# Performance work log

Hardware: AMD Instinct MI355X
Metric: run time of the kernel (lower is better)

The kernel has to match this reference:

```python
import jax, jax.numpy as jnp
import numpy as np

N_HEAD = 4
N_BIT = 8      # ssm coder bits, table_len = 2**8 = 256
IN_DIM = 8
FFN_V = 4      # ffn coder bits, 2**4 = 16 codes per head
FFN_DEPTH = 8  # tree depth, 2**8 = 256 leaves
TBL = 2 ** N_BIT


def _bern(key, logits):
    # torch.bernoulli(logits.sigmoid())
    return jax.random.uniform(key, logits.shape) < jax.nn.sigmoid(logits)


def _bool2long(x, n):
    mul = (2 ** (n - 1 - jnp.arange(n))).astype(jnp.int32)
    return (x.astype(jnp.int32) * mul).sum(-1)


def _long2bool(x, n):
    mul = (2 ** (n - 1 - jnp.arange(n))).astype(jnp.int32)
    return ((x[..., None] // mul) % 2).astype(bool)


def _tree_ffn(q, qs, key_p, val_p, rng):
    # q: (N, Q) bool, qs: (N, Q) float  (qs broadcast per head, matching intent)
    N, Q = q.shape
    H, depth = N_HEAD, FFN_DEPTH
    nv = 2 ** depth
    nk = nv - 1
    qf = jnp.broadcast_to(q[:, None, :], (N, H, Q)).reshape(N * H, Q)
    qs = jnp.broadcast_to(qs[:, None, :], (N, H, Q)).reshape(N * H, Q)
    qs = (2.0 * qf.astype(qs.dtype) - 1.0) * qs
    ix_h = jnp.arange(N * H, dtype=jnp.int32) % H
    ix = jnp.zeros(N * H, dtype=jnp.int32)
    key_flat = key_p.reshape(-1, 2 * Q)  # (H*nk, 2Q)
    support = None
    for d in range(depth):
        ix_k = ix_h * nk + (2 ** d - 1) + ix
        kw = key_flat[ix_k]  # (NH, 2Q)
        kb = _bern(jax.random.fold_in(rng, d), kw).reshape(-1, Q, 2)
        k1 = kb[:, :, 0].astype(qs.dtype)
        k2 = kb[:, :, 1].astype(qs.dtype)
        k1 = -jnp.logaddexp(-k1, qs)
        k2 = -jnp.logaddexp(-k2, -qs)
        lor_s = jnp.logaddexp(k1, k2)
        lor_s = -jax.nn.logsumexp(-lor_s, axis=-1)  # (NH,)
        lor = _bern(jax.random.fold_in(rng, 100 + d), lor_s)
        lor_s = (2.0 * lor.astype(qs.dtype) - 1.0) * lor_s
        ix = 2 * ix + lor.astype(jnp.int32)
        support = lor_s if support is None else -jnp.logaddexp(-support, -lor_s)
    vw = val_p.reshape(-1, val_p.shape[-1])[ix_h * nv + ix]  # (NH, V)
    vb = _bern(jax.random.fold_in(rng, 999), vw)
    vs = (2.0 * vb.astype(qs.dtype) - 1.0) * vw
    vs = -jnp.logaddexp(-vs, -support[:, None])
    return vb.reshape(N, H, -1), vs.reshape(N, H, -1)


def _forward(x, xs, ffn_key, ffn_value, table, state0):
    rng = jax.random.key(42)
    B, L, D = x.shape
    H, V, T = N_HEAD, FFN_V, TBL
    xb, xss = _tree_ffn(x.reshape(-1, D), xs.reshape(-1, D), ffn_key, ffn_value,
                        jax.random.fold_in(rng, 1))
    xb = xb.reshape(B, L, H, V)
    xss = xss.reshape(B, L, H, V)
    xcode = _bool2long(xb, V)                      # (B,L,H) in [0,16)
    xss = -jax.nn.logsumexp(-xss, axis=-1)         # (B,L,H)
    # sample stochastic lookup tables, independently per batch element
    tlog = jnp.broadcast_to(table, (B,) + table.shape[1:])  # (B,64,T,8)
    tb = _bern(jax.random.fold_in(rng, 2), tlog)
    table_s = table * (2.0 * tb.astype(xs.dtype) - 1.0)
    tcode = _bool2long(tb, N_BIT)                  # (B,64,T) in [0,T)
    table_s = -jax.nn.logsumexp(-table_s, axis=-1) # (B,64,T)
    head_off = (jnp.arange(L * H, dtype=jnp.int32) % H) * (2 ** V)
    idx = xcode.reshape(B, L * H) + head_off[None, :]
    y = jnp.take_along_axis(tcode, idx[:, :, None], axis=1).reshape(B, L, H, T)
    ys = jnp.take_along_axis(table_s, idx[:, :, None], axis=1).reshape(B, L, H, T)
    ys = -jnp.logaddexp(-ys, -xss[..., None])
    # Blelloch-style doubling scan; compose = table gather + soft-AND in log domain
    i = 1
    while i < L:
        y1 = y[:, :L - i]
        z = jnp.take_along_axis(y[:, i:], y1, axis=-1)
        zs = -jnp.logaddexp(-ys[:, :L - i], -jnp.take_along_axis(ys[:, i:], y1, axis=-1))
        y = jnp.concatenate([y[:, :i], z], axis=1)
        ys = jnp.concatenate([ys[:, :i], zs], axis=1)
        i *= 2
    # initial state
    s0b = _bern(jax.random.fold_in(rng, 3), jnp.broadcast_to(state0, (B,) + state0.shape[1:]))
    s0s = state0 * (2.0 * s0b.astype(xs.dtype) - 1.0)  # (B,H,8)
    s0 = _bool2long(s0b, N_BIT)                        # (B,H)
    s0s = -jax.nn.logsumexp(-s0s, axis=-1)             # (B,H)
    sidx = jnp.broadcast_to(s0[:, None, :, None], (B, L, H, 1))
    z = jnp.take_along_axis(y, sidx, axis=-1)[..., 0]   # (B,L,H)
    zs = jnp.take_along_axis(ys, sidx, axis=-1)[..., 0]
    zs = -jnp.logaddexp(-s0s[:, None, :], -zs)
    zb = _long2bool(z, N_BIT)                           # (B,L,H,8)
    zs = jnp.broadcast_to(zs[..., None], zb.shape)
    return zb.reshape(B, L, H * N_BIT), zs.reshape(B, L, H * N_BIT)


def setup_inputs() -> dict:
    key = jax.random.key(0)
    k = jax.random.split(key, 6)
    B, L = 8, 4096
    x = jax.random.randint(k[0], (B, L, IN_DIM), 0, 2).astype(bool)
    xs = jax.random.normal(k[1], (B, L, IN_DIM), dtype=jnp.float32)
    ffn_key = jax.random.normal(k[2], (N_HEAD, 2 ** FFN_DEPTH - 1, 2 * IN_DIM), dtype=jnp.float32) + 3.0
    ffn_value = jax.random.normal(k[3], (N_HEAD, 2 ** FFN_DEPTH, FFN_V), dtype=jnp.float32) + 3.0
    table = jax.random.normal(k[4], (1, (2 ** FFN_V) * N_HEAD, TBL, N_BIT), dtype=jnp.float32)
    state0 = jax.random.normal(k[5], (1, N_HEAD, N_BIT), dtype=jnp.float32)
    return {"x": x, "xs": xs, "ffn_key": ffn_key, "ffn_value": ffn_value,
            "table": table, "state0": state0}


def reference(x, xs, ffn_key, ffn_value, table, state0):
    return _forward(x, xs, ffn_key, ffn_value, table, state0)
```

## Files before the change

### kernel.cpp

```cpp
#include <hip/hip_runtime.h>
#include <hip/hip_bf16.h>
#include <stdint.h>
#include <math.h>

#define BB 8
#define LL 4096
#define HH 4
#define DD 8
#define VV 4
#define DEPTH 8
#define TBLN 256
#define NBIT 8
#define NROW 131072
#define CHUNK 64
#define NCHUNK 64

#define PARTITIONABLE 1
#define MATH_XLA_CPU 1

__device__ __forceinline__ uint32_t rotl32(uint32_t v, int r){ return (v<<r)|(v>>(32-r)); }

__device__ __forceinline__ void tf2x32(uint32_t k0, uint32_t k1, uint32_t x0, uint32_t x1,
                                       uint32_t& o0, uint32_t& o1){
  uint32_t ks2 = k0 ^ k1 ^ 0x1BD11BDAu;
  x0 += k0; x1 += k1;
  x0+=x1; x1=rotl32(x1,13); x1^=x0;
  x0+=x1; x1=rotl32(x1,15); x1^=x0;
  x0+=x1; x1=rotl32(x1,26); x1^=x0;
  x0+=x1; x1=rotl32(x1, 6); x1^=x0;
  x0+=k1; x1+=ks2+1u;
  x0+=x1; x1=rotl32(x1,17); x1^=x0;
  x0+=x1; x1=rotl32(x1,29); x1^=x0;
  x0+=x1; x1=rotl32(x1,16); x1^=x0;
  x0+=x1; x1=rotl32(x1,24); x1^=x0;
  x0+=ks2; x1+=k0+2u;
  x0+=x1; x1=rotl32(x1,13); x1^=x0;
  x0+=x1; x1=rotl32(x1,15); x1^=x0;
  x0+=x1; x1=rotl32(x1,26); x1^=x0;
  x0+=x1; x1=rotl32(x1, 6); x1^=x0;
  x0+=k0; x1+=k1+3u;
  x0+=x1; x1=rotl32(x1,17); x1^=x0;
  x0+=x1; x1=rotl32(x1,29); x1^=x0;
  x0+=x1; x1=rotl32(x1,16); x1^=x0;
  x0+=x1; x1=rotl32(x1,24); x1^=x0;
  x0+=k1; x1+=ks2+4u;
  x0+=x1; x1=rotl32(x1,13); x1^=x0;
  x0+=x1; x1=rotl32(x1,15); x1^=x0;
  x0+=x1; x1=rotl32(x1,26); x1^=x0;
  x0+=x1; x1=rotl32(x1, 6); x1^=x0;
  x0+=ks2; x1+=k0+5u;
  o0 = x0; o1 = x1;
}

struct K2 { uint32_t a, b; };
__device__ __forceinline__ K2 kfold(K2 k, uint32_t d){
  K2 r; tf2x32(k.a, k.b, 0u, d, r.a, r.b); return r;
}

__device__ __forceinline__ uint32_t rbits(K2 k, uint32_t p, uint32_t n){
#if PARTITIONABLE
  uint32_t o0, o1; tf2x32(k.a, k.b, 0u, p, o0, o1); return o0 ^ o1;
#else
  uint32_t half = n >> 1;
  uint32_t o0, o1;
  if (p < half){ tf2x32(k.a, k.b, p, p + half, o0, o1); return o0; }
  else         { tf2x32(k.a, k.b, p - half, p, o0, o1); return o1; }
#endif
}

__device__ __forceinline__ float bits2u(uint32_t b){
  return __uint_as_float((b >> 9) | 0x3f800000u) - 1.0f;
}

__device__ __forceinline__ float xla_expf(float x){
#if MATH_XLA_CPU
  #pragma clang fp contract(off)
  const float exp_hi = 88.3762626647950f;
  const float exp_lo = -88.3762626647949f;
  const float log2e  = 1.44269504088896341f;
  const float c1 = 0.693359375f;
  const float c2 = -2.12194440e-4f;
  float xc = fmaxf(fminf(x, exp_hi), exp_lo);
  float fx = floorf(xc * log2e + 0.5f);
  float tmp = fx * c1;
  float z1  = fx * c2;
  float r = xc - tmp;
  r = r - z1;
  float z = r * r;
  float y = 1.9875691500E-4f;
  y = y * r + 1.3981999507E-3f;
  y = y * r + 8.3334519073E-3f;
  y = y * r + 4.1665795894E-2f;
  y = y * r + 1.6666665459E-1f;
  y = y * r + 5.0000001201E-1f;
  y = y * z + r;
  y = y + 1.0f;
  int emm0 = (int)fx + 127;
  float scale = __int_as_float(emm0 << 23);
  return fmaxf(y * scale, x);
#else
  return expf(x);
#endif
}

__device__ __forceinline__ float xla_logf(float a){
#if MATH_XLA_CPU
  #pragma clang fp contract(off)
  float x = fmaxf(a, __uint_as_float(0x00800000u));
  uint32_t bits = __float_as_uint(x);
  int em = (int)(bits >> 23) - 126;
  x = __uint_as_float((bits & 0x007fffffu) | 0x3f000000u);
  float e = (float)em;
  bool mlt = x < 0.707106781186547524f;
  float tmp1 = mlt ? x : 0.0f;
  float xm = x - 1.0f;
  e = e - (mlt ? 1.0f : 0.0f);
  xm = xm + tmp1;
  float z = xm * xm;
  float y = 7.0376836292E-2f;
  y = y * xm + (-1.1514610310E-1f);
  y = y * xm + 1.1676998740E-1f;
  y = y * xm + (-1.2420140846E-1f);
  y = y * xm + 1.4249322787E-1f;
  y = y * xm + (-1.6668057665E-1f);
  y = y * xm + 2.0000714765E-1f;
  y = y * xm + (-2.4999993993E-1f);
  y = y * xm + 3.3333331174E-1f;
  y = y * xm;
  y = y * z;
  y = e * (-2.12194440e-4f) + y;
  y = y - 0.5f * z;
  float res = xm + y;
  res = e * 0.693359375f + res;
  return res;
#else
  return logf(a);
#endif
}

__device__ __forceinline__ float xla_log1pf(float x){
#if MATH_XLA_CPU
  #pragma clang fp contract(off)
  if (fabsf(x) < 1e-4f){
    return ((-0.5f * x) + 1.0f) * x;
  }
  return xla_logf(1.0f + x);
#else
  return log1pf(x);
#endif
}

__device__ __forceinline__ float xla_logaddexp(float a, float b){
  #pragma clang fp contract(off)
  float m = fmaxf(a, b);
  float d = a - b;
  return m + xla_log1pf(xla_expf(-fabsf(d)));
}

template<int NV>
__device__ __forceinline__ float neg_lse_neg(const float* v){
  #pragma clang fp contract(off)
  float m = -v[0];
  #pragma unroll
  for (int i = 1; i < NV; i++) m = fmaxf(m, -v[i]);
  float s = 0.f;
  #pragma unroll
  for (int i = 0; i < NV; i++) s = s + xla_expf((-v[i]) - m);
  return -(xla_logf(s) + m);
}

__device__ __forceinline__ bool bern_bit(float u, float w){
  #pragma clang fp contract(off)
  float e = xla_expf(-w);
  float s = 1.0f / (1.0f + e);
  return u < s;
}

__device__ __forceinline__ float andf(float a, float b){
  float na = -a, nb = -b;
  float m = fmaxf(na, nb);
  float d = fabsf(na - nb);
  return -(m + log1pf(expf(-d)));
}
#define AND_IDENT 1e30f

__global__ void k_init(const uint32_t* xw, int* flag,
                       const float* s0w, int* s0code, float* s0s){
  __shared__ int any;
  if (threadIdx.x == 0) any = 0;
  __syncthreads();
  int bad = 0;
  for (int i = threadIdx.x; i < 1024; i += 256){
    uint32_t w = xw[i];
    if (w != 0u && w != 1u && w != 0x3F800000u) bad = 1;
  }
  if (bad) atomicOr(&any, 1);
  __syncthreads();
  if (threadIdx.x == 0) *flag = any;

  int t = threadIdx.x;
  if (t < 32){
    int b = t >> 2, h = t & 3;
    K2 root{0u, 42u};
    K2 sk = kfold(root, 3u);
    float v[NBIT];
    uint32_t code = 0;
    #pragma unroll
    for (int j = 0; j < NBIT; j++){
      float w = s0w[h*NBIT + j];
      uint32_t p = (uint32_t)((b*4 + h)*NBIT + j);
      float u = bits2u(rbits(sk, p, 256u));
      bool bit = bern_bit(u, w);
      code |= (bit ? 1u : 0u) << (NBIT - 1 - j);
      v[j] = bit ? w : -w;
    }
    s0code[t] = (int)code;
    s0s[t]    = neg_lse_neg<NBIT>(v);
  }
}

__global__ __launch_bounds__(256) void k_ffn(const void* xraw, const float* xs,
                                             const float* fk, const float* fv,
                                             uint8_t* xcode, float* xss, const int* flag){
  int r = blockIdx.x * blockDim.x + threadIdx.x;
  if (r >= NROW) return;
  int n = r >> 2;
  int h = r & 3;
  bool u8mode = (*flag != 0);
  const uint8_t* x8   = (const uint8_t*)xraw;
  const uint32_t* x32 = (const uint32_t*)xraw;

  float qs[DD];
  #pragma unroll
  for (int j = 0; j < DD; j++){
    bool qb = u8mode ? (x8[n*DD + j] != 0) : (x32[n*DD + j] != 0u);
    float v = xs[n*DD + j];
    qs[j] = qb ? v : -v;
  }

  K2 root{0u, 42u};
  K2 rngT = kfold(root, 1u);

  uint32_t ix = 0;
  float support = 0.f;
  for (int d = 0; d < DEPTH; d++){
    K2 kd = kfold(rngT, (uint32_t)d);
    const float* kw = fk + (size_t)(h*255 + (1<<d) - 1 + (int)ix) * 16;
    float lor[DD];
    #pragma unroll
    for (int j = 0; j < DD; j++){
      uint32_t p1 = (uint32_t)r * 16u + 2u*(uint32_t)j;
      float u1 = bits2u(rbits(kd, p1,      2097152u));
      float u2 = bits2u(rbits(kd, p1 + 1u, 2097152u));
      float b1 = bern_bit(u1, kw[2*j])     ? 1.f : 0.f;
      float b2 = bern_bit(u2, kw[2*j + 1]) ? 1.f : 0.f;
      float k1 = -xla_logaddexp(-b1,  qs[j]);
      float k2 = -xla_logaddexp(-b2, -qs[j]);
      lor[j] = xla_logaddexp(k1, k2);
    }
    float lor_s = neg_lse_neg<DD>(lor);
    K2 lk = kfold(rngT, 100u + (uint32_t)d);
    float ul = bits2u(rbits(lk, (uint32_t)r, 131072u));
    bool lb = bern_bit(ul, lor_s);
    float ls = lb ? lor_s : -lor_s;
    ix = 2u*ix + (lb ? 1u : 0u);
    support = (d == 0) ? ls : -xla_logaddexp(-support, -ls);
  }

  K2 vk = kfold(rngT, 999u);
  const float* vw = fv + (size_t)(h*256 + (int)ix) * VV;
  float vs[VV];
  uint32_t code = 0;
  #pragma unroll
  for (int c = 0; c < VV; c++){
    float u = bits2u(rbits(vk, (uint32_t)r*4u + (uint32_t)c, 524288u));
    bool b = bern_bit(u, vw[c]);
    code |= (b ? 1u : 0u) << (VV - 1 - c);
    float sv = b ? vw[c] : -vw[c];
    vs[c] = -xla_logaddexp(-sv, -support);
  }
  xcode[r] = (uint8_t)code;
  xss[r]   = neg_lse_neg<VV>(vs);
}

__global__ __launch_bounds__(256) void k_table(const float* table, uint8_t* tcode, float* tabs){
  int idx = blockIdx.x * blockDim.x + threadIdx.x;
  if (idx >= 131072) return;
  int rem = idx & 16383;
  K2 root{0u, 42u};
  K2 tk = kfold(root, 2u);
  float v[NBIT];
  uint32_t code = 0;
  #pragma unroll
  for (int j = 0; j < NBIT; j++){
    float w = table[(size_t)rem * NBIT + j];
    uint32_t p = (uint32_t)idx * 8u + (uint32_t)j;
    float u = bits2u(rbits(tk, p, 1048576u));
    bool bit = bern_bit(u, w);
    code |= (bit ? 1u : 0u) << (NBIT - 1 - j);
    v[j] = bit ? w : -w;
  }
  tcode[idx] = (uint8_t)code;
  tabs[idx]  = neg_lse_neg<NBIT>(v);
}

__global__ __launch_bounds__(256) void k_A(const uint8_t* tcode, const uint8_t* xcode,
                                           uint8_t* F){
  int blk = blockIdx.x;
  int c  = blk & 63;
  int bh = blk >> 6;
  int b = bh >> 2, h = bh & 3;
  __shared__ int4 sT4[256];
  __shared__ uint8_t sXC[CHUNK];
  uint8_t* sT = (uint8_t*)sT4;
  int t = threadIdx.x;
  const int rowbase = (b*64 + h*16) * 256;
  sT4[t] = ((const int4*)(tcode + rowbase))[t];
  if (t < CHUNK){
    int l = c*CHUNK + t;
    sXC[t] = xcode[(b*LL + l)*HH + h];
  }
  __syncthreads();
  int cur = t;
  #pragma unroll 8
  for (int k = 0; k < CHUNK; k++){
    cur = sT[(int)sXC[k]*256 + cur];
  }
  F[(size_t)blk*256 + t] = (uint8_t)cur;
}

__global__ __launch_bounds__(256) void k_B(const uint8_t* F, const int* s0code, int* carryZ){
  int bh = blockIdx.x;
  __shared__ int4 sF4[1024];
  uint8_t* sF = (uint8_t*)sF4;
  int t = threadIdx.x;
  const int4* src = (const int4*)(F + (size_t)bh*16384);
  for (int i = t; i < 1024; i += 256) sF4[i] = src[i];
  __syncthreads();
  if (t == 0){
    int z = s0code[bh];
    for (int c = 0; c < NCHUNK; c++){ carryZ[bh*NCHUNK + c] = z; z = sF[c*256 + z]; }
  }
}

__global__ __launch_bounds__(64) void k_C1(const uint8_t* tcode, const float* tabs,
                                           const uint8_t* xcode, const float* xss,
                                           const int* carryZ,
                                           uint8_t* zOut, float* P, float* T){
  int blk = blockIdx.x;
  int c  = blk & 63;
  int bh = blk >> 6;
  int b = bh >> 2, h = bh & 3;
  __shared__ int4 sT4[256];
  uint8_t* sT = (uint8_t*)sT4;
  int t = threadIdx.x;
  const int rowbase = (b*64 + h*16) * 256;
  const int4* src = (const int4*)(tcode + rowbase);
  #pragma unroll
  for (int i = 0; i < 4; i++) sT4[t + 64*i] = src[t + 64*i];

  int l = c*CHUNK + t;
  int r = (b*LL + l)*HH + h;
  int   xcv = xcode[r];
  float xsv = xss[r];
  __syncthreads();

  int z = carryZ[blk];
  int aReg = 0, zReg = 0;
  for (int k = 0; k < CHUNK; k++){
    int xck = __shfl(xcv, k, 64);
    int a = xck*256 + z;
    z = sT[a];
    if (t == k){ aReg = a; zReg = z; }
  }

  float p = andf(tabs[rowbase + aReg], xsv);
  #pragma unroll
  for (int off = 1; off < 64; off <<= 1){
    float o = __shfl_up(p, off, 64);
    if (t >= off) p = andf(o, p);
  }
  zOut[blk*CHUNK + t] = (uint8_t)zReg;
  P[blk*CHUNK + t] = p;
  if (t == 63) T[blk] = p;
}

__global__ __launch_bounds__(256) void k_C2(const uint8_t* zOut, const float* P,
                                            const float* T, const float* s0s,
                                            float* out){
  int blk = blockIdx.x;
  int c = blk & 63;
  int b = blk >> 6;
  __shared__ float carryL[4];
  int t = threadIdx.x;
  int w = t >> 6, lane = t & 63;

  float val = (lane < c) ? T[(b*4 + w)*64 + lane] : AND_IDENT;
  #pragma unroll
  for (int off = 1; off < 64; off <<= 1){
    float o = __shfl_xor(val, off, 64);
    val = andf(val, o);
  }
  float carry = andf(val, s0s[b*4 + w]);
  if (lane == 0) carryL[w] = carry;
  __syncthreads();

  int k = t >> 2, h = t & 3;
  int cblk = (b*4 + h)*64 + c;
  int z = zOut[cblk*CHUNK + k];
  float sc = andf(carryL[h], P[cblk*CHUNK + k]);

  size_t base = (size_t)blk*2048 + (size_t)t*8;
  float4 b0, b1;
  b0.x = (float)((z >> 7) & 1); b0.y = (float)((z >> 6) & 1);
  b0.z = (float)((z >> 5) & 1); b0.w = (float)((z >> 4) & 1);
  b1.x = (float)((z >> 3) & 1); b1.y = (float)((z >> 2) & 1);
  b1.z = (float)((z >> 1) & 1); b1.w = (float)( z       & 1);
  float4 s4; s4.x = sc; s4.y = sc; s4.z = sc; s4.w = sc;
  *(float4*)(out + base)     = b0;
  *(float4*)(out + base + 4) = b1;
  *(float4*)(out + 1048576 + base)     = s4;
  *(float4*)(out + 1048576 + base + 4) = s4;
}

extern "C" void kernel_launch(void* const* d_in, const int* in_sizes, int n_in,
                              void* d_out, int out_size, void* d_ws, size_t ws_size,
                              hipStream_t stream) {
  const void*  x      = d_in[0];
  const float* xs     = (const float*)d_in[1];
  const float* fk     = (const float*)d_in[2];
  const float* fv     = (const float*)d_in[3];
  const float* table  = (const float*)d_in[4];
  const float* s0w    = (const float*)d_in[5];
  float* out          = (float*)d_out;

  uint8_t* ws = (uint8_t*)d_ws;
  uint8_t* xcode_ = ws;
  uint8_t* tcode_ = ws + 131072;
  uint8_t* F_     = ws + 262144;
  float*   xss_   = (float*)(ws + 786432);
  float*   tabs_  = (float*)(ws + 1310720);
  uint8_t* zOut_  = ws + 1835008;
  float*   P_     = (float*)(ws + 1966080);
  float*   T_     = (float*)(ws + 2490368);
  int*     carryZ_= (int*)  (ws + 2498560);
  int*     s0code_= (int*)  (ws + 2506752);
  float*   s0s_   = (float*)(ws + 2506880);
  int*     flag_  = (int*)  (ws + 2507008);

  k_init <<<1, 256, 0, stream>>>((const uint32_t*)x, flag_, s0w, s0code_, s0s_);
  k_ffn  <<<NROW/256, 256, 0, stream>>>(x, xs, fk, fv, xcode_, xss_, flag_);
  k_table<<<131072/256, 256, 0, stream>>>(table, tcode_, tabs_);
  k_A    <<<32*NCHUNK, 256, 0, stream>>>(tcode_, xcode_, F_);
  k_B    <<<32, 256, 0, stream>>>(F_, s0code_, carryZ_);
  k_C1   <<<32*NCHUNK, 64, 0, stream>>>(tcode_, tabs_, xcode_, xss_, carryZ_, zOut_, P_, T_);
  k_C2   <<<BB*NCHUNK, 256, 0, stream>>>(zOut_, P_, T_, s0s_, out);
}
```

Measured before the change: 204.7 us.

## Precompute sigmoids, RNG keys and per-bit logaddexp tables outside the tree loop

A new pre-pass kernel computes sigmoid of the table, ffn_key and ffn_value weights once, and derives the per-depth threefry fold keys once into a small buffer. The tree FFN precomputes, per input position, the four possible lor values (key bits 0/1 x 0/1), so each depth step only selects among them instead of evaluating three logaddexps per element. The table kernel uses vectorized float4 loads and compares against the precomputed sigmoids. This removes repeated exp/log and hash work in the hot kernels, at the cost of extra workspace traffic and one extra pass over the table.

```diff
diff --git a/kernel.cpp b/kernel.cpp
--- a/kernel.cpp
+++ b/kernel.cpp
@@ -9,7 +9,6 @@
 #define DD 8
 #define VV 4
 #define DEPTH 8
-#define TBLN 256
 #define NBIT 8
 #define NROW 131072
 #define CHUNK 64
@@ -57,14 +56,9 @@
   K2 r; tf2x32(k.a, k.b, 0u, d, r.a, r.b); return r;
 }
 
-__device__ __forceinline__ uint32_t rbits(K2 k, uint32_t p, uint32_t n){
+__device__ __forceinline__ uint32_t rbits(K2 k, uint32_t p){
 #if PARTITIONABLE
   uint32_t o0, o1; tf2x32(k.a, k.b, 0u, p, o0, o1); return o0 ^ o1;
-#else
-  uint32_t half = n >> 1;
-  uint32_t o0, o1;
-  if (p < half){ tf2x32(k.a, k.b, p, p + half, o0, o1); return o0; }
-  else         { tf2x32(k.a, k.b, p - half, p, o0, o1); return o1; }
 #endif
 }
 
@@ -73,7 +67,6 @@
 }
 
 __device__ __forceinline__ float xla_expf(float x){
-#if MATH_XLA_CPU
   #pragma clang fp contract(off)
   const float exp_hi = 88.3762626647950f;
   const float exp_lo = -88.3762626647949f;
@@ -98,13 +91,9 @@
   int emm0 = (int)fx + 127;
   float scale = __int_as_float(emm0 << 23);
   return fmaxf(y * scale, x);
-#else
-  return expf(x);
-#endif
 }
 
 __device__ __forceinline__ float xla_logf(float a){
-#if MATH_XLA_CPU
   #pragma clang fp contract(off)
   float x = fmaxf(a, __uint_as_float(0x00800000u));
   uint32_t bits = __float_as_uint(x);
@@ -133,21 +122,14 @@
   float res = xm + y;
   res = e * 0.693359375f + res;
   return res;
-#else
-  return logf(a);
-#endif
 }
 
 __device__ __forceinline__ float xla_log1pf(float x){
-#if MATH_XLA_CPU
   #pragma clang fp contract(off)
   if (fabsf(x) < 1e-4f){
     return ((-0.5f * x) + 1.0f) * x;
   }
   return xla_logf(1.0f + x);
-#else
-  return log1pf(x);
-#endif
 }
 
 __device__ __forceinline__ float xla_logaddexp(float a, float b){
@@ -169,11 +151,10 @@
   return -(xla_logf(s) + m);
 }
 
-__device__ __forceinline__ bool bern_bit(float u, float w){
+__device__ __forceinline__ float xla_sigmoid(float w){
   #pragma clang fp contract(off)
   float e = xla_expf(-w);
-  float s = 1.0f / (1.0f + e);
-  return u < s;
+  return 1.0f / (1.0f + e);
 }
 
 __device__ __forceinline__ float andf(float a, float b){
@@ -184,43 +165,66 @@
 }
 #define AND_IDENT 1e30f
 
-__global__ void k_init(const uint32_t* xw, int* flag,
-                       const float* s0w, int* s0code, float* s0s){
-  __shared__ int any;
-  if (threadIdx.x == 0) any = 0;
-  __syncthreads();
-  int bad = 0;
-  for (int i = threadIdx.x; i < 1024; i += 256){
-    uint32_t w = xw[i];
-    if (w != 0u && w != 1u && w != 0x3F800000u) bad = 1;
-  }
-  if (bad) atomicOr(&any, 1);
-  __syncthreads();
-  if (threadIdx.x == 0) *flag = any;
-
-  int t = threadIdx.x;
-  if (t < 32){
-    int b = t >> 2, h = t & 3;
-    K2 root{0u, 42u};
-    K2 sk = kfold(root, 3u);
-    float v[NBIT];
-    uint32_t code = 0;
-    #pragma unroll
-    for (int j = 0; j < NBIT; j++){
-      float w = s0w[h*NBIT + j];
-      uint32_t p = (uint32_t)((b*4 + h)*NBIT + j);
-      float u = bits2u(rbits(sk, p, 256u));
-      bool bit = bern_bit(u, w);
-      code |= (bit ? 1u : 0u) << (NBIT - 1 - j);
-      v[j] = bit ? w : -w;
+__global__ __launch_bounds__(256) void k_pre(const uint32_t* xw, int* flag,
+                      const float* s0w, int* s0code, float* s0s,
+                      const float* fk, const float* fv, const float* table,
+                      float* sigT, float* sigFK, float* sigFV, uint32_t* keys){
+  int i = blockIdx.x * 256 + threadIdx.x;
+  if (i < 131072)              sigT [i]          = xla_sigmoid(table[i]);
+  else if (i < 131072+16320)   sigFK[i-131072]   = xla_sigmoid(fk[i-131072]);
+  else if (i < 131072+16320+4096) sigFV[i-131072-16320] = xla_sigmoid(fv[i-131072-16320]);
+
+  if (blockIdx.x == 0){
+    __shared__ int any;
+    int t = threadIdx.x;
+    if (t == 0) any = 0;
+    __syncthreads();
+    int bad = 0;
+    for (int k = t; k < 1024; k += 256){
+      uint32_t w = xw[k];
+      if (w != 0u && w != 1u && w != 0x3F800000u) bad = 1;
     }
-    s0code[t] = (int)code;
-    s0s[t]    = neg_lse_neg<NBIT>(v);
+    if (bad) atomicOr(&any, 1);
+    __syncthreads();
+    if (t == 0) *flag = any;
+
+    if (t < 32){
+      int b = t >> 2, h = t & 3;
+      K2 root{0u, 42u};
+      K2 sk = kfold(root, 3u);
+      float v[NBIT];
+      uint32_t code = 0;
+      #pragma unroll
+      for (int j = 0; j < NBIT; j++){
+        float w = s0w[h*NBIT + j];
+        uint32_t p = (uint32_t)((b*4 + h)*NBIT + j);
+        float u = bits2u(rbits(sk, p));
+        bool bit = u < xla_sigmoid(w);
+        code |= (bit ? 1u : 0u) << (NBIT - 1 - j);
+        v[j] = bit ? w : -w;
+      }
+      s0code[t] = (int)code;
+      s0s[t]    = neg_lse_neg<NBIT>(v);
+    }
+    if (t == 0){
+      K2 root{0u, 42u};
+      K2 rngT = kfold(root, 1u);
+      for (int d = 0; d < DEPTH; d++){
+        K2 kd = kfold(rngT, (uint32_t)d);
+        keys[2*d] = kd.a; keys[2*d+1] = kd.b;
+        K2 lk = kfold(rngT, 100u + (uint32_t)d);
+        keys[16+2*d] = lk.a; keys[16+2*d+1] = lk.b;
+      }
+      K2 vk = kfold(rngT, 999u);
+      keys[32] = vk.a; keys[33] = vk.b;
+    }
   }
 }
 
 __global__ __launch_bounds__(256) void k_ffn(const void* xraw, const float* xs,
-                                             const float* fk, const float* fv,
+                                             const float* sigFK,
+                                             const float* fv, const float* sigFV,
+                                             const uint32_t* keys,
                                              uint8_t* xcode, float* xss, const int* flag){
   int r = blockIdx.x * blockDim.x + threadIdx.x;
   if (r >= NROW) return;
@@ -230,51 +234,57 @@
   const uint8_t* x8   = (const uint8_t*)xraw;
   const uint32_t* x32 = (const uint32_t*)xraw;
 
-  float qs[DD];
+  float L0[DD], L1[DD], L2[DD], L3[DD];
   #pragma unroll
   for (int j = 0; j < DD; j++){
     bool qb = u8mode ? (x8[n*DD + j] != 0) : (x32[n*DD + j] != 0u);
     float v = xs[n*DD + j];
-    qs[j] = qb ? v : -v;
-  }
-
-  K2 root{0u, 42u};
-  K2 rngT = kfold(root, 1u);
+    float q = qb ? v : -v;
+    float A0 = -xla_logaddexp(-0.0f, q);
+    float A1 = -xla_logaddexp(-1.0f, q);
+    float B0 = -xla_logaddexp(-0.0f, -q);
+    float B1 = -xla_logaddexp(-1.0f, -q);
+    L0[j] = xla_logaddexp(A0, B0);
+    L1[j] = xla_logaddexp(A1, B0);
+    L2[j] = xla_logaddexp(A0, B1);
+    L3[j] = xla_logaddexp(A1, B1);
+  }
 
   uint32_t ix = 0;
   float support = 0.f;
   for (int d = 0; d < DEPTH; d++){
-    K2 kd = kfold(rngT, (uint32_t)d);
-    const float* kw = fk + (size_t)(h*255 + (1<<d) - 1 + (int)ix) * 16;
+    K2 kd{keys[2*d], keys[2*d+1]};
+    const float* skw = sigFK + (size_t)(h*255 + (1<<d) - 1 + (int)ix) * 16;
     float lor[DD];
     #pragma unroll
     for (int j = 0; j < DD; j++){
       uint32_t p1 = (uint32_t)r * 16u + 2u*(uint32_t)j;
-      float u1 = bits2u(rbits(kd, p1,      2097152u));
-      float u2 = bits2u(rbits(kd, p1 + 1u, 2097152u));
-      float b1 = bern_bit(u1, kw[2*j])     ? 1.f : 0.f;
-      float b2 = bern_bit(u2, kw[2*j + 1]) ? 1.f : 0.f;
-      float k1 = -xla_logaddexp(-b1,  qs[j]);
-      float k2 = -xla_logaddexp(-b2, -qs[j]);
-      lor[j] = xla_logaddexp(k1, k2);
+      float u1 = bits2u(rbits(kd, p1));
+      float u2 = bits2u(rbits(kd, p1 + 1u));
+      bool b1 = u1 < skw[2*j];
+      bool b2 = u2 < skw[2*j + 1];
+      float t01 = b1 ? L1[j] : L0[j];
+      float t23 = b1 ? L3[j] : L2[j];
+      lor[j] = b2 ? t23 : t01;
     }
     float lor_s = neg_lse_neg<DD>(lor);
-    K2 lk = kfold(rngT, 100u + (uint32_t)d);
-    float ul = bits2u(rbits(lk, (uint32_t)r, 131072u));
-    bool lb = bern_bit(ul, lor_s);
+    K2 lk{keys[16+2*d], keys[16+2*d+1]};
+    float ul = bits2u(rbits(lk, (uint32_t)r));
+    bool lb = ul < xla_sigmoid(lor_s);
     float ls = lb ? lor_s : -lor_s;
     ix = 2u*ix + (lb ? 1u : 0u);
     support = (d == 0) ? ls : -xla_logaddexp(-support, -ls);
   }
 
-  K2 vk = kfold(rngT, 999u);
-  const float* vw = fv + (size_t)(h*256 + (int)ix) * VV;
+  K2 vk{keys[32], keys[33]};
+  const float* vw  = fv    + (size_t)(h*256 + (int)ix) * VV;
+  const float* svw = sigFV + (size_t)(h*256 + (int)ix) * VV;
   float vs[VV];
   uint32_t code = 0;
   #pragma unroll
   for (int c = 0; c < VV; c++){
-    float u = bits2u(rbits(vk, (uint32_t)r*4u + (uint32_t)c, 524288u));
-    bool b = bern_bit(u, vw[c]);
+    float u = bits2u(rbits(vk, (uint32_t)r*4u + (uint32_t)c));
+    bool b = u < svw[c];
     code |= (b ? 1u : 0u) << (VV - 1 - c);
     float sv = b ? vw[c] : -vw[c];
     vs[c] = -xla_logaddexp(-sv, -support);
@@ -283,22 +293,27 @@
   xss[r]   = neg_lse_neg<VV>(vs);
 }
 
-__global__ __launch_bounds__(256) void k_table(const float* table, uint8_t* tcode, float* tabs){
+__global__ __launch_bounds__(256) void k_table(const float* table, const float* sigT,
+                                               uint8_t* tcode, float* tabs){
   int idx = blockIdx.x * blockDim.x + threadIdx.x;
   if (idx >= 131072) return;
   int rem = idx & 16383;
   K2 root{0u, 42u};
   K2 tk = kfold(root, 2u);
+  float4 w0 = *(const float4*)(table + (size_t)rem*NBIT);
+  float4 w1 = *(const float4*)(table + (size_t)rem*NBIT + 4);
+  float4 g0 = *(const float4*)(sigT  + (size_t)rem*NBIT);
+  float4 g1 = *(const float4*)(sigT  + (size_t)rem*NBIT + 4);
+  float w[NBIT] = {w0.x,w0.y,w0.z,w0.w,w1.x,w1.y,w1.z,w1.w};
+  float g[NBIT] = {g0.x,g0.y,g0.z,g0.w,g1.x,g1.y,g1.z,g1.w};
   float v[NBIT];
   uint32_t code = 0;
   #pragma unroll
   for (int j = 0; j < NBIT; j++){
-    float w = table[(size_t)rem * NBIT + j];
-    uint32_t p = (uint32_t)idx * 8u + (uint32_t)j;
-    float u = bits2u(rbits(tk, p, 1048576u));
-    bool bit = bern_bit(u, w);
+    float u = bits2u(rbits(tk, (uint32_t)idx * 8u + (uint32_t)j));
+    bool bit = u < g[j];
     code |= (bit ? 1u : 0u) << (NBIT - 1 - j);
-    v[j] = bit ? w : -w;
+    v[j] = bit ? w[j] : -w[j];
   }
   tcode[idx] = (uint8_t)code;
   tabs[idx]  = neg_lse_neg<NBIT>(v);
@@ -447,10 +462,15 @@
   int*     s0code_= (int*)  (ws + 2506752);
   float*   s0s_   = (float*)(ws + 2506880);
   int*     flag_  = (int*)  (ws + 2507008);
-
-  k_init <<<1, 256, 0, stream>>>((const uint32_t*)x, flag_, s0w, s0code_, s0s_);
-  k_ffn  <<<NROW/256, 256, 0, stream>>>(x, xs, fk, fv, xcode_, xss_, flag_);
-  k_table<<<131072/256, 256, 0, stream>>>(table, tcode_, tabs_);
+  float*   sigT_  = (float*)(ws + 2507264);
+  float*   sigFK_ = (float*)(ws + 3031552);
+  float*   sigFV_ = (float*)(ws + 3096832);
+  uint32_t* keys_ = (uint32_t*)(ws + 3113216);
+
+  k_pre  <<<592, 256, 0, stream>>>((const uint32_t*)x, flag_, s0w, s0code_, s0s_,
+                                   fk, fv, table, sigT_, sigFK_, sigFV_, keys_);
+  k_ffn  <<<NROW/256, 256, 0, stream>>>(x, xs, sigFK_, fv, sigFV_, keys_, xcode_, xss_, flag_);
+  k_table<<<131072/256, 256, 0, stream>>>(table, sigT_, tcode_, tabs_);
   k_A    <<<32*NCHUNK, 256, 0, stream>>>(tcode_, xcode_, F_);
   k_B    <<<32, 256, 0, stream>>>(F_, s0code_, carryZ_);
   k_C1   <<<32*NCHUNK, 64, 0, stream>>>(tcode_, tabs_, xcode_, xss_, carryZ_, zOut_, P_, T_);
```

New measurement: 254.3 us. 24.2% more time.
